# Optimization experiments

Hardware: AMD Instinct MI355X
Metric: run time of the kernel (lower is better)

## Reference

```python
import jax, jax.numpy as jnp
import numpy as np

LAMBDA_1 = 1.0
LAMBDA_2 = 0.5


def setup_inputs() -> dict:
    key = jax.random.key(0)
    k1, k2, k3, k4, k5 = jax.random.split(key, 5)
    N_TRAIN, N_UNL, C = 4096, 32768, 1000
    G, K = 512, 64
    return {
        "train_logits": jax.random.normal(k1, (N_TRAIN, C), dtype=jnp.float32),
        "train_targets": jax.random.randint(k2, (N_TRAIN,), 0, C, dtype=jnp.int64),
        "unlabeled_logits": jax.random.normal(k3, (N_UNL, C), dtype=jnp.float32),
        "centroid_ids": jax.random.randint(k4, (G,), 0, N_TRAIN, dtype=jnp.int64),
        "member_ids": jax.random.randint(k5, (G, K), 0, N_UNL, dtype=jnp.int64),
    }


def reference(train_logits, train_targets, unlabeled_logits, centroid_ids, member_ids):
    N_unl = unlabeled_logits.shape[0]
    G, K = member_ids.shape

    # --- cross-entropy (mean) ---
    logp = jax.nn.log_softmax(train_logits, axis=-1)
    ce = -jnp.mean(jnp.take_along_axis(logp, train_targets[:, None], axis=1))

    # --- gather group tensors ---
    centroids = train_logits[centroid_ids]          # [G, C]
    members = unlabeled_logits[member_ids]          # [G, K, C]

    # --- alignment: sum_g sum_k ||centroid_g - member_gk||_2 / N_unl ---
    align = jnp.sum(jnp.linalg.norm(centroids[:, None, :] - members, axis=-1)) / N_unl

    # --- robustness: per-group upper-triangle pairwise L2 sums / (K * N_unl) ---
    sq = jnp.sum(members * members, axis=-1)                       # [G, K]
    gram = jnp.einsum("gkc,glc->gkl", members, members)            # [G, K, K]
    d2 = jnp.maximum(sq[:, :, None] + sq[:, None, :] - 2.0 * gram, 0.0)
    dist = jnp.sqrt(jnp.where(d2 > 0, d2, 1.0)) * (d2 > 0)         # safe sqrt
    iu = jnp.triu(jnp.ones((K, K), dtype=dist.dtype), k=1)         # i < j pairs
    robust = jnp.sum(dist * iu) / (K * N_unl)

    return ce + LAMBDA_1 * align + LAMBDA_2 * robust
```

## Files before the change

kernel.cpp:

```cpp
#include <hip/hip_runtime.h>

#define N_TRAIN 4096
#define N_UNL   32768
#define C_DIM   1000
#define G_GRP   512
#define K_MEM   64

#define CE_BLOCKS (N_TRAIN / 16)
#define NBLK      (G_GRP + CE_BLOCKS)

#define CHUNKS  8
#define CCOLS   128
#define PITCH_B 272
#define ROWS    65

typedef short        short8 __attribute__((ext_vector_type(8)));
typedef float        f32x4  __attribute__((ext_vector_type(4)));
typedef unsigned int u32x2  __attribute__((ext_vector_type(2)));

__device__ __forceinline__ unsigned int pack_bf(float a, float b) {
    unsigned int ua = __float_as_uint(a) + 0x8000u;
    unsigned int ub = __float_as_uint(b) + 0x8000u;
    return (ua >> 16) | (ub & 0xffff0000u);
}

__device__ __forceinline__ void lds_barrier() {
    asm volatile("s_waitcnt lgkmcnt(0)" ::: "memory");
    __builtin_amdgcn_s_barrier();
}

__global__ __launch_bounds__(256, 3) void fused_kernel(const float* __restrict__ train,
                                                       const int*   __restrict__ targets,
                                                       const float* __restrict__ unl,
                                                       const int*   __restrict__ cids,
                                                       const int*   __restrict__ mids,
                                                       float* __restrict__ out) {
    __shared__ __align__(16) unsigned short bf[2][ROWS * (PITCH_B / 2)];
    __shared__ int   ids_sh[K_MEM];
    __shared__ float sq_sh[K_MEM];
    __shared__ float red_sh[4];
    __shared__ float sqc_sh;

    const int tid  = threadIdx.x;
    const int w    = tid >> 6;
    const int lane = tid & 63;

    if (blockIdx.x >= G_GRP) {
        const int blk = (int)blockIdx.x - G_GRP;
        float ce = 0.f;
        for (int r4 = 0; r4 < 4; ++r4) {
            const int row = blk * 16 + w * 4 + r4;
            const float* rp = train + (long)row * C_DIM;
            float4 x[4];
#pragma unroll
            for (int i = 0; i < 4; ++i) {
                const int cb = lane * 4 + i * 256;
                x[i] = (cb < C_DIM) ? *(const float4*)(rp + cb)
                                    : make_float4(-1e30f, -1e30f, -1e30f, -1e30f);
            }
            float m = fmaxf(fmaxf(x[0].x, x[0].y), fmaxf(x[0].z, x[0].w));
#pragma unroll
            for (int i = 1; i < 4; ++i)
                m = fmaxf(m, fmaxf(fmaxf(x[i].x, x[i].y), fmaxf(x[i].z, x[i].w)));
#pragma unroll
            for (int off = 32; off > 0; off >>= 1) m = fmaxf(m, __shfl_xor(m, off, 64));
            float s = 0.f;
#pragma unroll
            for (int i = 0; i < 4; ++i)
                s += __expf(x[i].x - m) + __expf(x[i].y - m) +
                     __expf(x[i].z - m) + __expf(x[i].w - m);
#pragma unroll
            for (int off = 32; off > 0; off >>= 1) s += __shfl_xor(s, off, 64);
            if (lane == 0) {
                int t = targets[row];
                ce += -(rp[t] - m - __logf(s));
            }
        }
        if (lane == 0) red_sh[w] = ce;
        __syncthreads();
        if (tid == 0)
            atomicAdd(out, (red_sh[0] + red_sh[1] + red_sh[2] + red_sh[3]) *
                           (1.0f / (float)N_TRAIN));
        return;
    }

    const int g    = blockIdx.x;
    const int quad = lane >> 4;
    const int c16  = lane & 15;

    if (tid < K_MEM) ids_sh[tid] = mids[g * K_MEM + tid];
    __syncthreads();

    unsigned int roff[16];
#pragma unroll
    for (int i = 0; i < 16; ++i)
        roff[i] = (unsigned int)ids_sh[w * 16 + i] * (unsigned int)(C_DIM * 4);
    const unsigned int coff = (unsigned int)cids[g] * (unsigned int)(C_DIM * 4);
    const char* const ubase = (const char*)unl;
    const char* const tbase = (const char*)train;

    f32x4 acc[4], accC, accD;
#pragma unroll
    for (int t = 0; t < 4; ++t) acc[t] = (f32x4){0.f, 0.f, 0.f, 0.f};
    accC = (f32x4){0.f, 0.f, 0.f, 0.f};
    accD = (f32x4){0.f, 0.f, 0.f, 0.f};

    const float4 z4 = make_float4(0.f, 0.f, 0.f, 0.f);

    float4 regs[16];
    float4 creg;

    {
        const long ob = (long)lane * 16;
#pragma unroll
        for (int i = 0; i < 16; ++i)
            regs[i] = *(const float4*)(ubase + roff[i] + ob);
        if (w == 3) creg = *(const float4*)(tbase + coff + ob);
    }

#pragma unroll
    for (int ch = 0; ch < CHUNKS; ++ch) {
        unsigned short* const bufp = bf[ch & 1];
        const int l32 = lane & 31;
        if ((ch & 1) == 0 ? (lane < 32) : (lane >= 32)) {
#pragma unroll
            for (int i = 0; i < 16; ++i) {
                u32x2 h = {pack_bf(regs[i].x, regs[i].y), pack_bf(regs[i].z, regs[i].w)};
                *(u32x2*)((char*)bufp + (w * 16 + i) * PITCH_B + l32 * 8) = h;
            }
            if (w == 3) {
                u32x2 h = {pack_bf(creg.x, creg.y), pack_bf(creg.z, creg.w)};
                *(u32x2*)((char*)bufp + 64 * PITCH_B + l32 * 8) = h;
            }
        }
        if ((ch & 1) == 1 && ch + 1 < CHUNKS) {
            const int  sc = (ch + 1) >> 1;
            const int  cb = sc * 256 + lane * 4;
            const bool v  = (cb < C_DIM);
            const long ob = (long)cb * 4;
#pragma unroll
            for (int i = 0; i < 16; ++i)
                regs[i] = v ? *(const float4*)(ubase + roff[i] + ob) : z4;
            if (w == 3) creg = v ? *(const float4*)(tbase + coff + ob) : z4;
        }
        lds_barrier();
        __builtin_amdgcn_s_setprio(1);
#pragma unroll
        for (int s = 0; s < 4; ++s) {
            const int   kbb  = s * 64 + quad * 16;
            const char* base = (const char*)bufp;
            short8 b0 = *(const short8*)(base + (0 * 16 + c16) * PITCH_B + kbb);
            short8 b1 = *(const short8*)(base + (1 * 16 + c16) * PITCH_B + kbb);
            short8 b2 = *(const short8*)(base + (2 * 16 + c16) * PITCH_B + kbb);
            short8 b3 = *(const short8*)(base + (3 * 16 + c16) * PITCH_B + kbb);
            short8 aM = *(const short8*)(base + (w * 16 + c16) * PITCH_B + kbb);
            short8 bC = *(const short8*)(base + 64 * PITCH_B + kbb);
            acc[0] = __builtin_amdgcn_mfma_f32_16x16x32_bf16(aM, b0, acc[0], 0, 0, 0);
            acc[1] = __builtin_amdgcn_mfma_f32_16x16x32_bf16(aM, b1, acc[1], 0, 0, 0);
            acc[2] = __builtin_amdgcn_mfma_f32_16x16x32_bf16(aM, b2, acc[2], 0, 0, 0);
            acc[3] = __builtin_amdgcn_mfma_f32_16x16x32_bf16(aM, b3, acc[3], 0, 0, 0);
            accC = __builtin_amdgcn_mfma_f32_16x16x32_bf16(aM, bC, accC, 0, 0, 0);
            if (w == 0)
                accD = __builtin_amdgcn_mfma_f32_16x16x32_bf16(bC, bC, accD, 0, 0, 0);
        }
        __builtin_amdgcn_s_setprio(0);
    }

#pragma unroll
    for (int t = 0; t < 4; ++t) {
        if (t == w) {
#pragma unroll
            for (int r = 0; r < 4; ++r)
                if (c16 == quad * 4 + r) sq_sh[w * 16 + c16] = acc[t][r];
        }
    }
    if (tid == 0) sqc_sh = accD[0];
    __syncthreads();

    float local = 0.f;
    if (c16 == 0) {
#pragma unroll
        for (int r = 0; r < 4; ++r) {
            const int j = w * 16 + quad * 4 + r;
            const float d2 = sqc_sh + sq_sh[j] - 2.f * accC[r];
            if (d2 > 0.f) local += sqrtf(d2) * (1.0f / (float)N_UNL);
        }
    }
#pragma unroll
    for (int t = 0; t < 4; ++t) {
#pragma unroll
        for (int r = 0; r < 4; ++r) {
            const int i = w * 16 + quad * 4 + r;
            const int j = t * 16 + c16;
            if (j > i) {
                const float d2 = sq_sh[i] + sq_sh[j] - 2.f * acc[t][r];
                if (d2 > 0.f)
                    local += sqrtf(d2) * (0.5f / ((float)K_MEM * (float)N_UNL));
            }
        }
    }

#pragma unroll
    for (int off = 32; off > 0; off >>= 1) local += __shfl_xor(local, off, 64);
    if (lane == 0) red_sh[w] = local;
    __syncthreads();
    if (tid == 0) atomicAdd(out, red_sh[0] + red_sh[1] + red_sh[2] + red_sh[3]);
}

extern "C" void kernel_launch(void* const* d_in, const int* in_sizes, int n_in,
                              void* d_out, int out_size, void* d_ws, size_t ws_size,
                              hipStream_t stream) {
    (void)in_sizes; (void)n_in; (void)d_ws; (void)ws_size;
    const float* train_logits  = (const float*)d_in[0];
    const int*   train_targets = (const int*)d_in[1];
    const float* unl           = (const float*)d_in[2];
    const int*   centroid_ids  = (const int*)d_in[3];
    const int*   member_ids    = (const int*)d_in[4];
    float* out = (float*)d_out;

    hipMemsetAsync(out, 0, (size_t)out_size * sizeof(float), stream);
    fused_kernel<<<NBLK, 256, 0, stream>>>(train_logits, train_targets, unl,
                                           centroid_ids, member_ids, out);
}
```

Before: 207.9 us.

## Redistribute member-row loads across half-waves to halve register staging and raise occupancy

Instead of each wave loading 16 rows of 256 columns and writing half per chunk, each group of 32 threads now loads 8 rows of 128 columns per chunk, prefetching the next chunk every iteration. This halves the float4 staging registers, and launch bounds go from 3 to 4 blocks per SIMD-level occupancy target. The aim is more resident blocks to hide gather latency, at the cost of smaller, more frequent prefetches with less lookahead per chunk.

```diff
diff --git a/kernel.cpp b/kernel.cpp
--- a/kernel.cpp
+++ b/kernel.cpp
@@ -29,7 +29,7 @@
     __builtin_amdgcn_s_barrier();
 }
 
-__global__ __launch_bounds__(256, 3) void fused_kernel(const float* __restrict__ train,
+__global__ __launch_bounds__(256, 4) void fused_kernel(const float* __restrict__ train,
                                                        const int*   __restrict__ targets,
                                                        const float* __restrict__ unl,
                                                        const int*   __restrict__ cids,
@@ -91,10 +91,13 @@
     if (tid < K_MEM) ids_sh[tid] = mids[g * K_MEM + tid];
     __syncthreads();
 
-    unsigned int roff[16];
-#pragma unroll
-    for (int i = 0; i < 16; ++i)
-        roff[i] = (unsigned int)ids_sh[w * 16 + i] * (unsigned int)(C_DIM * 4);
+    const int rgrp = tid >> 5;
+    const int l32  = tid & 31;
+
+    unsigned int roff[8];
+#pragma unroll
+    for (int i = 0; i < 8; ++i)
+        roff[i] = (unsigned int)ids_sh[rgrp + 8 * i] * (unsigned int)(C_DIM * 4);
     const unsigned int coff = (unsigned int)cids[g] * (unsigned int)(C_DIM * 4);
     const char* const ubase = (const char*)unl;
     const char* const tbase = (const char*)train;
@@ -107,41 +110,36 @@
 
     const float4 z4 = make_float4(0.f, 0.f, 0.f, 0.f);
 
-    float4 regs[16];
+    float4 mreg[8];
     float4 creg;
-
     {
-        const long ob = (long)lane * 16;
-#pragma unroll
-        for (int i = 0; i < 16; ++i)
-            regs[i] = *(const float4*)(ubase + roff[i] + ob);
-        if (w == 3) creg = *(const float4*)(tbase + coff + ob);
+        const unsigned int ob = (unsigned int)(l32 * 16);
+#pragma unroll
+        for (int i = 0; i < 8; ++i)
+            mreg[i] = *(const float4*)(ubase + (size_t)(roff[i] + ob));
+        if (tid < 32) creg = *(const float4*)(tbase + (size_t)(coff + ob));
     }
 
 #pragma unroll
     for (int ch = 0; ch < CHUNKS; ++ch) {
         unsigned short* const bufp = bf[ch & 1];
-        const int l32 = lane & 31;
-        if ((ch & 1) == 0 ? (lane < 32) : (lane >= 32)) {
-#pragma unroll
-            for (int i = 0; i < 16; ++i) {
-                u32x2 h = {pack_bf(regs[i].x, regs[i].y), pack_bf(regs[i].z, regs[i].w)};
-                *(u32x2*)((char*)bufp + (w * 16 + i) * PITCH_B + l32 * 8) = h;
-            }
-            if (w == 3) {
-                u32x2 h = {pack_bf(creg.x, creg.y), pack_bf(creg.z, creg.w)};
-                *(u32x2*)((char*)bufp + 64 * PITCH_B + l32 * 8) = h;
-            }
-        }
-        if ((ch & 1) == 1 && ch + 1 < CHUNKS) {
-            const int  sc = (ch + 1) >> 1;
-            const int  cb = sc * 256 + lane * 4;
-            const bool v  = (cb < C_DIM);
-            const long ob = (long)cb * 4;
-#pragma unroll
-            for (int i = 0; i < 16; ++i)
-                regs[i] = v ? *(const float4*)(ubase + roff[i] + ob) : z4;
-            if (w == 3) creg = v ? *(const float4*)(tbase + coff + ob) : z4;
+#pragma unroll
+        for (int i = 0; i < 8; ++i) {
+            u32x2 h = {pack_bf(mreg[i].x, mreg[i].y), pack_bf(mreg[i].z, mreg[i].w)};
+            *(u32x2*)((char*)bufp + (rgrp + 8 * i) * PITCH_B + l32 * 8) = h;
+        }
+        if (tid < 32) {
+            u32x2 h = {pack_bf(creg.x, creg.y), pack_bf(creg.z, creg.w)};
+            *(u32x2*)((char*)bufp + 64 * PITCH_B + tid * 8) = h;
+        }
+        if (ch + 1 < CHUNKS) {
+            const int  col = (ch + 1) * CCOLS + l32 * 4;
+            const bool v   = (col < C_DIM);
+            const unsigned int ob = (unsigned int)(col * 4);
+#pragma unroll
+            for (int i = 0; i < 8; ++i)
+                mreg[i] = v ? *(const float4*)(ubase + (size_t)(roff[i] + ob)) : z4;
+            if (tid < 32) creg = v ? *(const float4*)(tbase + (size_t)(coff + ob)) : z4;
         }
         lds_barrier();
         __builtin_amdgcn_s_setprio(1);
```

Result: no change. 204.3 us (-1.7%).
